# Kernel tuning notes

Measured on AMD Instinct MI355X. Metric: run time of the kernel, lower is better.

The kernel has to match this reference:

```python
import jax, jax.numpy as jnp
import numpy as np
import math

N, M = 100000, 12
F, NF, H = 128, 64, 8
D = F // H


def setup_inputs() -> dict:
    key = jax.random.key(0)
    ks = jax.random.split(key, 20)
    s = 0.02
    inp = {
        "atom_fea": jax.random.normal(ks[0], (N, F), jnp.float32),
        "nbr_fea": jax.random.normal(ks[1], (N, M, NF), jnp.float32),
        "nbr_fea_idx": jax.random.randint(ks[2], (N, M), 0, N, jnp.int64),
        "Wq": jax.random.normal(ks[3], (F, F), jnp.float32) * s,
        "bq": jnp.zeros((F,), jnp.float32),
        "Wk": jax.random.normal(ks[4], (F, F), jnp.float32) * s,
        "bk": jnp.zeros((F,), jnp.float32),
        "Wv": jax.random.normal(ks[5], (F, F), jnp.float32) * s,
        "bv": jnp.zeros((F,), jnp.float32),
        "Wn": jax.random.normal(ks[6], (NF, F), jnp.float32) * s,
        "bn": jnp.zeros((F,), jnp.float32),
        "Wo": jax.random.normal(ks[7], (F, F), jnp.float32) * s,
        "bo": jnp.zeros((F,), jnp.float32),
        "Wg": jax.random.normal(ks[8], (2 * F, 1), jnp.float32) * s,
        "bg": jnp.zeros((1,), jnp.float32),
        "gamma": jnp.ones((F,), jnp.float32),
        "beta": jnp.zeros((F,), jnp.float32),
    }
    return inp


def reference(atom_fea, nbr_fea, nbr_fea_idx, Wq, bq, Wk, bk, Wv, bv,
              Wn, bn, Wo, bo, Wg, bg, gamma, beta):
    residual = atom_fea
    # projections [N, F] -> [N, H, D]
    q = (atom_fea @ Wq + bq).reshape(N, H, D)
    k = (atom_fea @ Wk + bk).reshape(N, H, D)
    v = (atom_fea @ Wv + bv).reshape(N, H, D)
    # gather neighbor K/V: [N, M, H, D]
    nbr_t = (nbr_fea @ Wn + bn).reshape(N, M, H, D)
    nk = k[nbr_fea_idx] + nbr_t
    nv = v[nbr_fea_idx] + nbr_t
    # scores over neighbors, per head
    scores = jnp.einsum("nhd,nmhd->nmh", q, nk) / math.sqrt(D)
    w = jax.nn.softmax(scores, axis=1)  # softmax over M neighbors
    att = jnp.einsum("nmh,nmhd->nhd", w, nv).reshape(N, F)
    out = att @ Wo + bo
    gate = jax.nn.sigmoid(jnp.concatenate([out, residual], axis=-1) @ Wg + bg)
    out = gate * out + (1.0 - gate) * residual
    # layer norm (eps=1e-5, torch default)
    mu = jnp.mean(out, axis=-1, keepdims=True)
    var = jnp.var(out, axis=-1, keepdims=True)
    out = (out - mu) * jax.lax.rsqrt(var + 1e-5) * gamma + beta
    return out
```

## Files before the change

kernel.cpp:

```cpp
#include <hip/hip_runtime.h>
#include <math.h>

#define NATOM 100000
#define MNBR 12
#define FDIM 128
#define NFDIM 64

typedef __attribute__((ext_vector_type(8))) short bf16x8;
typedef __attribute__((ext_vector_type(4))) float f32x4;

__device__ inline unsigned short f2bf(float x) {
    union { float f; unsigned u; } v; v.f = x;
    unsigned r = v.u + 0x7FFFu + ((v.u >> 16) & 1u);
    return (unsigned short)(r >> 16);
}

__device__ inline void st4bf(short* p, float4 x) {
    unsigned lo = (unsigned)f2bf(x.x) | ((unsigned)f2bf(x.y) << 16);
    unsigned hi = (unsigned)f2bf(x.z) | ((unsigned)f2bf(x.w) << 16);
    *(uint2*)p = make_uint2(lo, hi);
}

__global__ __launch_bounds__(256) void pack_weights(
    const float* __restrict__ Wq, const float* __restrict__ Wk,
    const float* __restrict__ Wv, const float* __restrict__ Wn,
    const float* __restrict__ Wo,
    short* __restrict__ pk1, short* __restrict__ pk2, short* __restrict__ pk3)
{
    int g = blockIdx.x * 256 + threadIdx.x;
    if (g < 49152) {
        int fe = g >> 9;
        int r = g & 511;
        int lane = r >> 3, jj = r & 7;
        int s = fe & 3, f = fe >> 2;
        int ct = f & 7, mt = f >> 3;
        int k = s * 32 + (lane >> 4) * 8 + jj;
        int n = ct * 16 + (lane & 15);
        const float* W = (mt == 0) ? Wq : ((mt == 1) ? Wk : Wv);
        pk1[g] = (short)f2bf(W[k * 128 + n]);
    } else if (g < 57344) {
        int g2 = g - 49152;
        int fe = g2 >> 9;
        int r = g2 & 511;
        int lane = r >> 3, jj = r & 7;
        int s = fe & 1, ct = fe >> 1;
        int k = s * 32 + (lane >> 4) * 8 + jj;
        int n = ct * 16 + (lane & 15);
        pk2[g2] = (short)f2bf(Wn[k * 128 + n]);
    } else {
        int g3 = g - 57344;
        int fe = g3 >> 9;
        int r = g3 & 511;
        int lane = r >> 3, jj = r & 7;
        int s = fe & 3, ct = fe >> 2;
        int k = s * 32 + (lane >> 4) * 8 + jj;
        int n = ct * 16 + (lane & 15);
        pk3[g3] = (short)f2bf(Wo[k * 128 + n]);
    }
}

__global__ __launch_bounds__(256) void qkv_mfma(
    const float* __restrict__ atom_fea,
    const short* __restrict__ pk1,
    const float* __restrict__ bq, const float* __restrict__ bk,
    const float* __restrict__ bv,
    float* __restrict__ q, float* __restrict__ k, float* __restrict__ v)
{
    __shared__ short s_a[128 * 136];
    const int tid = threadIdx.x;
    const int base = blockIdx.x * 128;
#pragma unroll
    for (int e = 0; e < 16; ++e) {
        int f4 = e * 256 + tid;
        int row = f4 >> 5, c4 = f4 & 31;
        int atom = base + row;
        float4 x = make_float4(0.f, 0.f, 0.f, 0.f);
        if (atom < NATOM) x = *(const float4*)(atom_fea + (size_t)atom * 128 + c4 * 4);
        st4bf(&s_a[row * 136 + c4 * 4], x);
    }
    __syncthreads();

    const int lane = tid & 63, w = tid >> 6;
    const int quad = lane >> 4, j16 = lane & 15;

    for (int rt = 0; rt < 8; ++rt) {
        f32x4 acc[6];
#pragma unroll
        for (int fl = 0; fl < 6; ++fl) acc[fl] = (f32x4){0.f, 0.f, 0.f, 0.f};

        const short* arow = &s_a[(rt * 16 + j16) * 136];
#pragma unroll
        for (int s = 0; s < 4; ++s) {
            bf16x8 af = *(const bf16x8*)(arow + s * 32 + quad * 8);
            bf16x8 bfr[6];
#pragma unroll
            for (int fl = 0; fl < 6; ++fl)
                bfr[fl] = *(const bf16x8*)(pk1 + ((((w * 6 + fl) * 4 + s) * 64 + lane) << 3));
#pragma unroll
            for (int fl = 0; fl < 6; ++fl)
                acc[fl] = __builtin_amdgcn_mfma_f32_16x16x32_bf16(af, bfr[fl], acc[fl], 0, 0, 0);
        }
#pragma unroll
        for (int fl = 0; fl < 6; ++fl) {
            const int f = w * 6 + fl;
            const int mt = f >> 3, ct = f & 7;
            const int col = ct * 16 + j16;
            const float b = (mt == 0 ? bq : (mt == 1 ? bk : bv))[col];
            float* op = (mt == 0 ? q : (mt == 1 ? k : v));
#pragma unroll
            for (int r = 0; r < 4; ++r) {
                int atom = base + rt * 16 + quad * 4 + r;
                if (atom < NATOM) op[(size_t)atom * 128 + col] = acc[fl][r] + b;
            }
        }
    }
}

__global__ __launch_bounds__(256) void attn_mfma(
    const float* __restrict__ nbr_fea,
    const int*   __restrict__ nbr_idx,
    const short* __restrict__ pk2,
    const float* __restrict__ bn,
    float* qatt,
    const float* __restrict__ kbuf,
    const float* __restrict__ vbuf)
{
    __shared__ short s_a[8 * 16 * 72];
    const int tid = threadIdx.x;
    const long long blk = blockIdx.x;

    const float* gsrc = nbr_fea + blk * 6144;
#pragma unroll
    for (int e = 0; e < 6; ++e) {
        int f4 = e * 256 + tid;
        int r = f4 >> 4, c4 = f4 & 15;
        int a = r / 12, m = r - a * 12;
        int lrow = (m / 3) * 4 + (m % 3);
        float4 x = *(const float4*)(gsrc + (size_t)f4 * 4);
        st4bf(&s_a[(a * 16 + lrow) * 72 + c4 * 4], x);
    }
    {
        int prow = tid >> 3, c = tid & 7;
        int a = prow >> 2, qd = prow & 3;
        *(uint4*)&s_a[(a * 16 + qd * 4 + 3) * 72 + c * 8] = make_uint4(0, 0, 0, 0);
    }
    __syncthreads();

    const int lane = tid & 63, w = tid >> 6;
    const int quad = lane >> 4, j16 = lane & 15;

    bf16x8 bfr[2][2];
#pragma unroll
    for (int hh = 0; hh < 2; ++hh)
#pragma unroll
        for (int s = 0; s < 2; ++s) {
            int ct = w * 2 + hh;
            bfr[hh][s] = *(const bf16x8*)(pk2 + (((ct * 2 + s) * 64 + lane) << 3));
        }

    const float bnc0 = bn[w * 32 + j16];
    const float bnc1 = bn[w * 32 + 16 + j16];

#pragma unroll
    for (int a = 0; a < 8; ++a) {
        const long long n = blk * 8 + a;
        f32x4 acc0 = (f32x4){0.f, 0.f, 0.f, 0.f};
        f32x4 acc1 = (f32x4){0.f, 0.f, 0.f, 0.f};
#pragma unroll
        for (int s = 0; s < 2; ++s) {
            bf16x8 af = *(const bf16x8*)&s_a[(a * 16 + j16) * 72 + s * 32 + quad * 8];
            acc0 = __builtin_amdgcn_mfma_f32_16x16x32_bf16(af, bfr[0][s], acc0, 0, 0, 0);
            acc1 = __builtin_amdgcn_mfma_f32_16x16x32_bf16(af, bfr[1][s], acc1, 0, 0, 0);
        }
        int nidx[3];
#pragma unroll
        for (int r = 0; r < 3; ++r)
            nidx[r] = nbr_idx[n * 12 + quad * 3 + r];

#pragma unroll
        for (int hh = 0; hh < 2; ++hh) {
            const int col = w * 32 + hh * 16 + j16;
            const float bnc = hh ? bnc1 : bnc0;
            const f32x4 t = hh ? acc1 : acc0;
            const float qv = qatt[n * 128 + col];
            float sc[3], nv[3];
#pragma unroll
            for (int r = 0; r < 3; ++r) {
                float tm = t[r] + bnc;
                size_t off = (size_t)nidx[r] * 128 + col;
                float nk = kbuf[off] + tm;
                nv[r] = vbuf[off] + tm;
                float p = qv * nk;
                p += __shfl_xor(p, 1, 16);
                p += __shfl_xor(p, 2, 16);
                p += __shfl_xor(p, 4, 16);
                p += __shfl_xor(p, 8, 16);
                sc[r] = p * 0.25f;
            }
            float mx = fmaxf(fmaxf(sc[0], sc[1]), sc[2]);
            mx = fmaxf(mx, __shfl_xor(mx, 16));
            mx = fmaxf(mx, __shfl_xor(mx, 32));
            float es = 0.f, av = 0.f;
#pragma unroll
            for (int r = 0; r < 3; ++r) {
                float e = __expf(sc[r] - mx);
                es += e;
                av += e * nv[r];
            }
            es += __shfl_xor(es, 16); es += __shfl_xor(es, 32);
            av += __shfl_xor(av, 16); av += __shfl_xor(av, 32);
            if (quad == 0) qatt[n * 128 + col] = av / es;
        }
    }
}

__global__ __launch_bounds__(256) void out_mfma(
    const float* __restrict__ attb, const float* __restrict__ atom_fea,
    const short* __restrict__ pk3, const float* __restrict__ bo,
    const float* __restrict__ Wg, const float* __restrict__ bg,
    const float* __restrict__ gamma, const float* __restrict__ beta,
    float* __restrict__ out)
{
    __shared__ short s_a[64 * 136];
    __shared__ float s_o[64 * 132];
    const int tid = threadIdx.x;
    const int base = blockIdx.x * 64;
#pragma unroll
    for (int e = 0; e < 8; ++e) {
        int f4 = e * 256 + tid;
        int row = f4 >> 5, c4 = f4 & 31;
        int atom = base + row;
        float4 x = make_float4(0.f, 0.f, 0.f, 0.f);
        if (atom < NATOM) x = *(const float4*)(attb + (size_t)atom * 128 + c4 * 4);
        st4bf(&s_a[row * 136 + c4 * 4], x);
    }
    __syncthreads();

    const int lane = tid & 63, w = tid >> 6;
    const int quad = lane >> 4, j16 = lane & 15;

    f32x4 acc[8];
#pragma unroll
    for (int f = 0; f < 8; ++f) acc[f] = (f32x4){0.f, 0.f, 0.f, 0.f};

    const short* arow = &s_a[(w * 16 + j16) * 136];
#pragma unroll
    for (int s = 0; s < 4; ++s) {
        bf16x8 af = *(const bf16x8*)(arow + s * 32 + quad * 8);
        bf16x8 bfr[8];
#pragma unroll
        for (int f = 0; f < 8; ++f)
            bfr[f] = *(const bf16x8*)(pk3 + (((f * 4 + s) * 64 + lane) << 3));
#pragma unroll
        for (int f = 0; f < 8; ++f)
            acc[f] = __builtin_amdgcn_mfma_f32_16x16x32_bf16(af, bfr[f], acc[f], 0, 0, 0);
    }
#pragma unroll
    for (int f = 0; f < 8; ++f) {
        const int col = f * 16 + j16;
        const float b = bo[col];
#pragma unroll
        for (int r = 0; r < 4; ++r)
            s_o[(w * 16 + quad * 4 + r) * 132 + col] = acc[f][r] + b;
    }
    __syncthreads();

    const int g = tid >> 4;
    const int r16 = tid & 15;
    for (int p = 0; p < 4; ++p) {
        const int a_loc = p * 16 + g;
        const int atom = base + a_loc;
        const bool ok = (atom < NATOM);
        float o8[8], res8[8];
        float pg = 0.f;
#pragma unroll
        for (int tt = 0; tt < 8; ++tt) {
            int jj = r16 + tt * 16;
            o8[tt] = s_o[a_loc * 132 + jj];
            res8[tt] = ok ? atom_fea[(size_t)atom * 128 + jj] : 0.f;
            pg += o8[tt] * Wg[jj] + res8[tt] * Wg[128 + jj];
        }
        pg += __shfl_xor(pg, 1, 16);
        pg += __shfl_xor(pg, 2, 16);
        pg += __shfl_xor(pg, 4, 16);
        pg += __shfl_xor(pg, 8, 16);
        const float gt = 1.f / (1.f + __expf(-(pg + bg[0])));

        float s1 = 0.f, s2 = 0.f;
        float gv8[8];
#pragma unroll
        for (int tt = 0; tt < 8; ++tt) {
            float gv = gt * o8[tt] + (1.f - gt) * res8[tt];
            gv8[tt] = gv;
            s1 += gv; s2 += gv * gv;
        }
        s1 += __shfl_xor(s1, 1, 16); s2 += __shfl_xor(s2, 1, 16);
        s1 += __shfl_xor(s1, 2, 16); s2 += __shfl_xor(s2, 2, 16);
        s1 += __shfl_xor(s1, 4, 16); s2 += __shfl_xor(s2, 4, 16);
        s1 += __shfl_xor(s1, 8, 16); s2 += __shfl_xor(s2, 8, 16);
        const float mu = s1 * (1.f / 128.f);
        const float var = s2 * (1.f / 128.f) - mu * mu;
        const float rs = rsqrtf(var + 1e-5f);
        if (ok) {
#pragma unroll
            for (int tt = 0; tt < 8; ++tt) {
                int jj = r16 + tt * 16;
                out[(size_t)atom * 128 + jj] =
                    (gv8[tt] - mu) * rs * gamma[jj] + beta[jj];
            }
        }
    }
}

extern "C" void kernel_launch(void* const* d_in, const int* in_sizes, int n_in,
                              void* d_out, int out_size, void* d_ws, size_t ws_size,
                              hipStream_t stream) {
    const float* atom_fea = (const float*)d_in[0];
    const float* nbr_fea  = (const float*)d_in[1];
    const int*   nbr_idx  = (const int*)d_in[2];
    const float* Wq = (const float*)d_in[3];
    const float* bq = (const float*)d_in[4];
    const float* Wk = (const float*)d_in[5];
    const float* bk = (const float*)d_in[6];
    const float* Wv = (const float*)d_in[7];
    const float* bv = (const float*)d_in[8];
    const float* Wn = (const float*)d_in[9];
    const float* bn = (const float*)d_in[10];
    const float* Wo = (const float*)d_in[11];
    const float* bo = (const float*)d_in[12];
    const float* Wg = (const float*)d_in[13];
    const float* bg = (const float*)d_in[14];
    const float* gm = (const float*)d_in[15];
    const float* bt = (const float*)d_in[16];

    float* qbuf = (float*)d_ws;
    float* kbuf = qbuf + (size_t)NATOM * FDIM;
    float* vbuf = kbuf + (size_t)NATOM * FDIM;
    short* pk1  = (short*)(vbuf + (size_t)NATOM * FDIM);
    short* pk2  = pk1 + 49152;
    short* pk3  = pk2 + 8192;
    float* outp = (float*)d_out;

    pack_weights<<<288, 256, 0, stream>>>(Wq, Wk, Wv, Wn, Wo, pk1, pk2, pk3);
    qkv_mfma<<<(NATOM + 127) / 128, 256, 0, stream>>>(
        atom_fea, pk1, bq, bk, bv, qbuf, kbuf, vbuf);
    attn_mfma<<<NATOM / 8, 256, 0, stream>>>(
        nbr_fea, nbr_idx, pk2, bn, qbuf, kbuf, vbuf);
    out_mfma<<<(NATOM + 63) / 64, 256, 0, stream>>>(
        qbuf, atom_fea, pk3, bo, Wg, bg, gm, bt, outp);
}
```

Baseline: 717.0 us.

## Store q/k/v and attention output intermediates as bf16 instead of fp32

The q, k, v and attention-output workspaces become bf16, which halves the bytes written by the projection kernel, the bytes fetched by the neighbor gathers, and the bytes read by the output kernel. The attention kernel now stages each block's q rows in shared memory, issues the neighbor index loads before the MFMAs, and loads all k/v values ahead of the softmax math. The output kernel copies bf16 directly into shared memory with no conversion. This trades accuracy, since intermediates are rounded to bf16, for less memory traffic.

```diff
diff --git a/kernel.cpp b/kernel.cpp
--- a/kernel.cpp
+++ b/kernel.cpp
@@ -8,11 +8,17 @@
 
 typedef __attribute__((ext_vector_type(8))) short bf16x8;
 typedef __attribute__((ext_vector_type(4))) float f32x4;
-
-__device__ inline unsigned short f2bf(float x) {
+typedef unsigned short u16;
+
+__device__ inline u16 f2bf(float x) {
     union { float f; unsigned u; } v; v.f = x;
     unsigned r = v.u + 0x7FFFu + ((v.u >> 16) & 1u);
-    return (unsigned short)(r >> 16);
+    return (u16)(r >> 16);
+}
+
+__device__ inline float b2f(u16 u) {
+    union { unsigned u; float f; } v; v.u = ((unsigned)u) << 16;
+    return v.f;
 }
 
 __device__ inline void st4bf(short* p, float4 x) {
@@ -64,7 +70,7 @@
     const short* __restrict__ pk1,
     const float* __restrict__ bq, const float* __restrict__ bk,
     const float* __restrict__ bv,
-    float* __restrict__ q, float* __restrict__ k, float* __restrict__ v)
+    u16* __restrict__ q, u16* __restrict__ k, u16* __restrict__ v)
 {
     __shared__ short s_a[128 * 136];
     const int tid = threadIdx.x;
@@ -106,11 +112,11 @@
             const int mt = f >> 3, ct = f & 7;
             const int col = ct * 16 + j16;
             const float b = (mt == 0 ? bq : (mt == 1 ? bk : bv))[col];
-            float* op = (mt == 0 ? q : (mt == 1 ? k : v));
+            u16* op = (mt == 0 ? q : (mt == 1 ? k : v));
 #pragma unroll
             for (int r = 0; r < 4; ++r) {
                 int atom = base + rt * 16 + quad * 4 + r;
-                if (atom < NATOM) op[(size_t)atom * 128 + col] = acc[fl][r] + b;
+                if (atom < NATOM) op[(unsigned)atom * 128u + col] = f2bf(acc[fl][r] + b);
             }
         }
     }
@@ -121,11 +127,12 @@
     const int*   __restrict__ nbr_idx,
     const short* __restrict__ pk2,
     const float* __restrict__ bn,
-    float* qatt,
-    const float* __restrict__ kbuf,
-    const float* __restrict__ vbuf)
+    u16* qatt,
+    const u16* __restrict__ kbuf,
+    const u16* __restrict__ vbuf)
 {
     __shared__ short s_a[8 * 16 * 72];
+    __shared__ u16   s_q[8 * 128];
     const int tid = threadIdx.x;
     const long long blk = blockIdx.x;
 
@@ -144,6 +151,9 @@
         int a = prow >> 2, qd = prow & 3;
         *(uint4*)&s_a[(a * 16 + qd * 4 + 3) * 72 + c * 8] = make_uint4(0, 0, 0, 0);
     }
+    if (tid < 128) {
+        ((uint4*)s_q)[tid] = ((const uint4*)(qatt + (size_t)blk * 1024))[tid];
+    }
     __syncthreads();
 
     const int lane = tid & 63, w = tid >> 6;
@@ -160,10 +170,17 @@
 
     const float bnc0 = bn[w * 32 + j16];
     const float bnc1 = bn[w * 32 + 16 + j16];
+    const unsigned base8 = (unsigned)blk * 8u;
+    const int cb = w * 32 + j16;
 
 #pragma unroll
     for (int a = 0; a < 8; ++a) {
-        const long long n = blk * 8 + a;
+        const unsigned n = base8 + a;
+        int nidx[3];
+#pragma unroll
+        for (int r = 0; r < 3; ++r)
+            nidx[r] = nbr_idx[n * 12u + quad * 3 + r];
+
         f32x4 acc0 = (f32x4){0.f, 0.f, 0.f, 0.f};
         f32x4 acc1 = (f32x4){0.f, 0.f, 0.f, 0.f};
 #pragma unroll
@@ -172,24 +189,34 @@
             acc0 = __builtin_amdgcn_mfma_f32_16x16x32_bf16(af, bfr[0][s], acc0, 0, 0, 0);
             acc1 = __builtin_amdgcn_mfma_f32_16x16x32_bf16(af, bfr[1][s], acc1, 0, 0, 0);
         }
-        int nidx[3];
-#pragma unroll
-        for (int r = 0; r < 3; ++r)
-            nidx[r] = nbr_idx[n * 12 + quad * 3 + r];
-
+
+        unsigned off[3];
+#pragma unroll
+        for (int r = 0; r < 3; ++r) off[r] = ((unsigned)nidx[r]) << 7;
+
+        float kk[2][3], vv[2][3];
 #pragma unroll
         for (int hh = 0; hh < 2; ++hh) {
-            const int col = w * 32 + hh * 16 + j16;
+            const int c = cb + hh * 16;
+#pragma unroll
+            for (int r = 0; r < 3; ++r) {
+                kk[hh][r] = b2f(kbuf[off[r] + c]);
+                vv[hh][r] = b2f(vbuf[off[r] + c]);
+            }
+        }
+
+#pragma unroll
+        for (int hh = 0; hh < 2; ++hh) {
+            const int c = cb + hh * 16;
+            const float qv = b2f(s_q[a * 128 + c]);
             const float bnc = hh ? bnc1 : bnc0;
             const f32x4 t = hh ? acc1 : acc0;
-            const float qv = qatt[n * 128 + col];
             float sc[3], nv[3];
 #pragma unroll
             for (int r = 0; r < 3; ++r) {
                 float tm = t[r] + bnc;
-                size_t off = (size_t)nidx[r] * 128 + col;
-                float nk = kbuf[off] + tm;
-                nv[r] = vbuf[off] + tm;
+                float nk = kk[hh][r] + tm;
+                nv[r] = vv[hh][r] + tm;
                 float p = qv * nk;
                 p += __shfl_xor(p, 1, 16);
                 p += __shfl_xor(p, 2, 16);
@@ -209,13 +236,13 @@
             }
             es += __shfl_xor(es, 16); es += __shfl_xor(es, 32);
             av += __shfl_xor(av, 16); av += __shfl_xor(av, 32);
-            if (quad == 0) qatt[n * 128 + col] = av / es;
+            if (quad == 0) qatt[n * 128u + c] = f2bf(av * __builtin_amdgcn_rcpf(es));
         }
     }
 }
 
 __global__ __launch_bounds__(256) void out_mfma(
-    const float* __restrict__ attb, const float* __restrict__ atom_fea,
+    const u16* __restrict__ attb, const float* __restrict__ atom_fea,
     const short* __restrict__ pk3, const float* __restrict__ bo,
     const float* __restrict__ Wg, const float* __restrict__ bg,
     const float* __restrict__ gamma, const float* __restrict__ beta,
@@ -226,13 +253,13 @@
     const int tid = threadIdx.x;
     const int base = blockIdx.x * 64;
 #pragma unroll
-    for (int e = 0; e < 8; ++e) {
-        int f4 = e * 256 + tid;
-        int row = f4 >> 5, c4 = f4 & 31;
+    for (int e = 0; e < 4; ++e) {
+        int u = e * 256 + tid;
+        int row = u >> 4, c8 = u & 15;
         int atom = base + row;
-        float4 x = make_float4(0.f, 0.f, 0.f, 0.f);
-        if (atom < NATOM) x = *(const float4*)(attb + (size_t)atom * 128 + c4 * 4);
-        st4bf(&s_a[row * 136 + c4 * 4], x);
+        uint4 x = make_uint4(0, 0, 0, 0);
+        if (atom < NATOM) x = *(const uint4*)(attb + (size_t)atom * 128 + c8 * 8);
+        *(uint4*)&s_a[row * 136 + c8 * 8] = x;
     }
     __syncthreads();
 
@@ -333,12 +360,12 @@
     const float* gm = (const float*)d_in[15];
     const float* bt = (const float*)d_in[16];
 
-    float* qbuf = (float*)d_ws;
-    float* kbuf = qbuf + (size_t)NATOM * FDIM;
-    float* vbuf = kbuf + (size_t)NATOM * FDIM;
-    short* pk1  = (short*)(vbuf + (size_t)NATOM * FDIM);
-    short* pk2  = pk1 + 49152;
-    short* pk3  = pk2 + 8192;
+    u16* qbuf = (u16*)d_ws;
+    u16* kbuf = qbuf + (size_t)NATOM * FDIM;
+    u16* vbuf = kbuf + (size_t)NATOM * FDIM;
+    short* pk1 = (short*)(vbuf + (size_t)NATOM * FDIM);
+    short* pk2 = pk1 + 49152;
+    short* pk3 = pk2 + 8192;
     float* outp = (float*)d_out;
 
     pack_weights<<<288, 256, 0, stream>>>(Wq, Wk, Wv, Wn, Wo, pk1, pk2, pk3);
```

Result: faster. 667.0 us (-7.0%).
